# Optimization experiments

Hardware: AMD Instinct MI355X
Metric: run time of the kernel (lower is better)

The kernel has to match this reference:

```python
import jax, jax.numpy as jnp
import numpy as np
import itertools

B = 2          # batches
NB = 65536     # points per batch
G = 100        # voxel grid extent per axis
CIN = 32
COUT = 32
K3 = 27        # 3x3x3 kernel offsets
CENTER = 13    # (0,0,0) offset index


def setup_inputs() -> dict:
    rng = np.random.default_rng(0)
    grid = -np.ones((B, G, G, G), dtype=np.int64)
    coords = []
    for b in range(B):
        flat = np.sort(rng.choice(G ** 3, size=NB, replace=False))
        x = flat // (G * G)
        y = (flat // G) % G
        z = flat % G
        grid[b, x, y, z] = np.arange(NB) + b * NB
        coords.append(np.stack([np.full(NB, b), x, y, z], axis=1))
    C = np.concatenate(coords, axis=0)  # [N,4] batch,x,y,z (batch-contiguous)
    offs = np.array(list(itertools.product([-1, 0, 1], repeat=3)))  # [27,3], idx 13 == (0,0,0)
    nx = C[:, 1][:, None] + offs[:, 0][None]
    ny = C[:, 2][:, None] + offs[:, 1][None]
    nz = C[:, 3][:, None] + offs[:, 2][None]
    inb = (nx >= 0) & (nx < G) & (ny >= 0) & (ny < G) & (nz >= 0) & (nz < G)
    nb = grid[C[:, 0][:, None], np.clip(nx, 0, G - 1), np.clip(ny, 0, G - 1), np.clip(nz, 0, G - 1)]
    nbr = np.where(inb, nb, -1).astype(np.int32)  # [N,27], -1 = no neighbor voxel

    key = jax.random.key(0)
    k1, k2, k3, k4, k5 = jax.random.split(key, 5)
    scale = 1.0 / np.sqrt(K3 * CIN)
    return {
        "x_F": jax.random.normal(k1, (B * NB, CIN), dtype=jnp.float32),
        "W_ch": jax.random.normal(k2, (K3, CIN, COUT), dtype=jnp.float32) * scale,
        "b_ch": jax.random.normal(k3, (COUT,), dtype=jnp.float32) * 0.01,
        "W_dw": jax.random.normal(k4, (K3, COUT, COUT), dtype=jnp.float32) * scale,
        "b_dw": jax.random.normal(k5, (COUT,), dtype=jnp.float32) * 0.01,
        "nbr": jnp.asarray(nbr),
        "th": 1,
        "num_batches": B,
    }


def _sparse_conv(F, W, b, nbr, valid):
    # F:[N,Cin], W:[27,Cin,Cout], nbr:[N,27] (clamped gather + mask)
    idx = jnp.maximum(nbr, 0)
    g = jnp.where(valid[:, :, None], F[idx], 0.0)  # [N,27,Cin]
    out = jnp.einsum('nkc,kcd->nd', g, W)
    return out if b is None else out + b


def reference(x_F, W_ch, b_ch, W_dw, b_dw, nbr, th, num_batches):
    valid = nbr >= 0
    idx = jnp.maximum(nbr, 0)

    # Channel_code: 3x3x3 sparse conv with bias
    x = _sparse_conv(x_F, W_ch, b_ch, nbr, valid)  # [N,COUT]

    # correlation score: ones-kernel conv with center tap zeroed, over all channels
    s = x.sum(-1)  # [N]
    valid_nc = valid.at[:, CENTER].set(False)
    corr = jnp.where(valid_nc, s[idx], 0.0).sum(-1)
    corr_norm = (x * x).sum(-1)  # 1x1 ones-kernel conv on x*x
    corr = corr / corr_norm

    # per-batch topk -> strong/weak split (batch-contiguous equal-sized batches)
    N = x.shape[0]
    nb_pts = N // num_batches
    k = int(nb_pts * th / 3.21)
    corr_b = corr.reshape(num_batches, nb_pts)
    _, top_idx = jax.lax.top_k(corr_b, k)
    mask = jnp.zeros((num_batches, nb_pts), dtype=bool)
    mask = mask.at[jnp.arange(num_batches)[:, None], top_idx].set(True).reshape(-1)

    # dw conv restricted to the strong subset (neighbors must also be strong)
    valid_s = valid & mask[idx] & mask[:, None]
    strong = _sparse_conv(x, W_dw, b_dw, nbr, valid_s)

    # union: strong points take conv output, weak points keep x features
    union_F = jnp.where(mask[:, None], strong, x)
    return union_F + x  # out = out + x
```

## Files before the change

### kernel.cpp

```cpp
#include <hip/hip_runtime.h>

#define K3 27
#define CENTER 13
#define NC 32
#define NREP 32

__global__ __launch_bounds__(256) void conv1_kernel(
    const float* __restrict__ xF,
    const float* __restrict__ Wch,
    const float* __restrict__ bch,
    const int*   __restrict__ nbr,
    float*  __restrict__ xo,
    double* __restrict__ so,
    double* __restrict__ cno)
{
    __shared__ float Gs[2][256 * 32];
    const int t     = threadIdx.x;
    const int pbase = blockIdx.x << 8;
    const int dgu   = __builtin_amdgcn_readfirstlane(t >> 6);
    const int pp    = t & 63;
    const int sw    = pp & 7;
    const int tsw   = t & 7;

    float acc[4][8];
#pragma unroll
    for (int i = 0; i < 4; i++)
#pragma unroll
        for (int d = 0; d < 8; d++) acc[i][d] = 0.f;

    float4 stg[8];
    {
        const int j = nbr[(pbase + t) * K3];
        if (j >= 0) {
            const float4* src = (const float4*)(xF + (size_t)j * NC);
#pragma unroll
            for (int m = 0; m < 8; m++) stg[m] = src[m];
        } else {
            const float4 z = make_float4(0.f, 0.f, 0.f, 0.f);
#pragma unroll
            for (int m = 0; m < 8; m++) stg[m] = z;
        }
    }

    for (int k = 0; k < K3; k++) {
        const int cur = k & 1;
        {
            float4* dst = (float4*)(Gs[cur] + t * 32);
#pragma unroll
            for (int m = 0; m < 8; m++) dst[m ^ tsw] = stg[m];
        }
        __syncthreads();
        if (k + 1 < K3) {
            const int j = nbr[(pbase + t) * K3 + k + 1];
            if (j >= 0) {
                const float4* src = (const float4*)(xF + (size_t)j * NC);
#pragma unroll
                for (int m = 0; m < 8; m++) stg[m] = src[m];
            } else {
                const float4 z = make_float4(0.f, 0.f, 0.f, 0.f);
#pragma unroll
                for (int m = 0; m < 8; m++) stg[m] = z;
            }
        }
        const float* __restrict__ Wk = Wch + k * (NC * NC) + dgu * 8;
#pragma unroll
        for (int cc = 0; cc < 8; ++cc) {
            const float4 g0 = ((const float4*)(Gs[cur] + (pp      ) * 32))[cc ^ sw];
            const float4 g1 = ((const float4*)(Gs[cur] + (pp +  64) * 32))[cc ^ sw];
            const float4 g2 = ((const float4*)(Gs[cur] + (pp + 128) * 32))[cc ^ sw];
            const float4 g3 = ((const float4*)(Gs[cur] + (pp + 192) * 32))[cc ^ sw];
#pragma unroll
            for (int c4 = 0; c4 < 4; c4++) {
                const float* wr = Wk + (cc * 4 + c4) * NC;
                const float4 wa = ((const float4*)wr)[0];
                const float4 wb = ((const float4*)wr)[1];
                const float wv[8] = {wa.x, wa.y, wa.z, wa.w, wb.x, wb.y, wb.z, wb.w};
                const float gv[4] = {(&g0.x)[c4], (&g1.x)[c4], (&g2.x)[c4], (&g3.x)[c4]};
#pragma unroll
                for (int i = 0; i < 4; i++)
#pragma unroll
                    for (int d = 0; d < 8; d++)
                        acc[i][d] = fmaf(gv[i], wv[d], acc[i][d]);
            }
        }
        __syncthreads();
    }

#pragma unroll
    for (int d = 0; d < 8; d++) {
        const float bv = bch[dgu * 8 + d];
#pragma unroll
        for (int i = 0; i < 4; i++) acc[i][d] += bv;
    }
#pragma unroll
    for (int i = 0; i < 4; i++) {
        const int p = pp + 64 * i;
        float4* dst = (float4*)(Gs[0] + p * 32);
        dst[(dgu * 2    ) ^ sw] = make_float4(acc[i][0], acc[i][1], acc[i][2], acc[i][3]);
        dst[(dgu * 2 + 1) ^ sw] = make_float4(acc[i][4], acc[i][5], acc[i][6], acc[i][7]);
    }
    __syncthreads();
    {
        double sum = 0.0, sq = 0.0;
        const float4* row = (const float4*)(Gs[0] + t * 32);
#pragma unroll
        for (int m = 0; m < 8; m++) {
            const float4 v = row[m ^ tsw];
            sum += (double)v.x + (double)v.y + (double)v.z + (double)v.w;
            sq  += (double)v.x * v.x + (double)v.y * v.y + (double)v.z * v.z + (double)v.w * v.w;
        }
        so[pbase + t]  = sum;
        cno[pbase + t] = sq;
    }
    {
        float4* xout = (float4*)(xo + (size_t)pbase * NC);
#pragma unroll
        for (int f = 0; f < 8; f++) {
            const int idx = f * 256 + t;
            const int row = idx >> 3;
            const int m   = idx & 7;
            xout[idx] = ((const float4*)(Gs[0] + row * 32))[m ^ (row & 7)];
        }
    }
}

__global__ __launch_bounds__(256) void corr_hist_kernel(
    const double* __restrict__ s,
    const double* __restrict__ cn,
    const int*    __restrict__ nbr,
    unsigned*     __restrict__ key,
    unsigned*     __restrict__ rep,
    int NBpts, int N)
{
    __shared__ int nlds[256 * K3];
    const int t     = threadIdx.x;
    const int pbase = blockIdx.x * 256;
    {
        const int* g = nbr + (size_t)pbase * K3;
#pragma unroll
        for (int i = 0; i < K3; i++) nlds[i * 256 + t] = g[i * 256 + t];
    }
    __syncthreads();
    const int n = pbase + t;

    int jj[K3];
#pragma unroll
    for (int k = 0; k < K3; k++) jj[k] = nlds[t * K3 + k];

    double v[K3];
#pragma unroll
    for (int k = 0; k < K3; k++) {
        if (k == CENTER) continue;
        const int j  = jj[k];
        const int ja = (j < 0) ? 0 : j;
        const double val = s[ja];
        v[k] = (j < 0) ? 0.0 : val;
    }
    double a0 = 0.0, a1 = 0.0, a2 = 0.0, a3 = 0.0;
#pragma unroll
    for (int k = 0; k < K3; k++) {
        if (k == CENTER) continue;
        const int c = k & 3;
        if (c == 0) a0 += v[k];
        else if (c == 1) a1 += v[k];
        else if (c == 2) a2 += v[k];
        else a3 += v[k];
    }
    const double sum = (a0 + a1) + (a2 + a3);

    const float corr = (float)(sum / cn[n]);
    const unsigned uu = __float_as_uint(corr);
    const unsigned u  = (uu & 0x80000000u) ? ~uu : (uu | 0x80000000u);
    key[n] = u;
    const int b = n / NBpts;
    const unsigned r = (unsigned)blockIdx.x & (NREP - 1);
    atomicAdd(&rep[(size_t)r * (2u * 65536u) + (size_t)b * 65536u + (u >> 16)], 1u);
}

__global__ __launch_bounds__(256) void reduce_rep_kernel(
    const unsigned* __restrict__ rep,
    unsigned*       __restrict__ hist_sum)
{
    const int g = blockIdx.x * 256 + threadIdx.x;
    unsigned sum = 0;
#pragma unroll
    for (int r = 0; r < NREP; r++)
        sum += rep[(size_t)r * (2u * 65536u) + g];
    hist_sum[g] = sum;
}

__global__ __launch_bounds__(1024) void scan_hi_kernel(
    const unsigned* __restrict__ hist,
    const int*      __restrict__ thp,
    unsigned*       __restrict__ selhi,
    int*            __restrict__ selrk,
    int NBpts)
{
    __shared__ unsigned ss[1024];
    const int b = blockIdx.x;
    const int t = threadIdx.x;
    const unsigned* h = hist + (size_t)b * 65536u + t * 64;
    unsigned sum = 0;
#pragma unroll 8
    for (int i = 0; i < 64; i++) sum += h[i];
    ss[t] = sum;
    __syncthreads();
    for (int off = 1; off < 1024; off <<= 1) {
        unsigned v = (t + off < 1024) ? ss[t + off] : 0u;
        __syncthreads();
        ss[t] += v;
        __syncthreads();
    }
    int k = (int)((double)NBpts * (double)thp[0] / 3.21);
    if (k < 1) k = 1;
    if (k > NBpts) k = NBpts;
    unsigned run = ss[t] - sum;
    for (int i = 63; i >= 0; --i) {
        const unsigned c = h[i];
        if ((int)run < k && k <= (int)(run + c)) {
            selhi[b] = (unsigned)(t * 64 + i);
            selrk[b] = k - (int)run;
        }
        run += c;
    }
}

__global__ __launch_bounds__(256) void hist_lo_kernel(
    const unsigned* __restrict__ key,
    const unsigned* __restrict__ selhi,
    unsigned*       __restrict__ hist2,
    int NBpts, int N)
{
    const int n = blockIdx.x * 256 + threadIdx.x;
    if (n >= N) return;
    const int b = n / NBpts;
    const unsigned u = key[n];
    if ((u >> 16) == selhi[b])
        atomicAdd(&hist2[(size_t)b * 65536u + (u & 0xFFFFu)], 1u);
}

__global__ __launch_bounds__(1024) void scan_lo_kernel(
    const unsigned* __restrict__ hist2,
    const unsigned* __restrict__ selhi,
    const int*      __restrict__ selrk,
    unsigned*       __restrict__ selT,
    int*            __restrict__ selr)
{
    __shared__ unsigned ss[1024];
    const int b = blockIdx.x;
    const int t = threadIdx.x;
    const unsigned* h = hist2 + (size_t)b * 65536u + t * 64;
    unsigned sum = 0;
#pragma unroll 8
    for (int i = 0; i < 64; i++) sum += h[i];
    ss[t] = sum;
    __syncthreads();
    for (int off = 1; off < 1024; off <<= 1) {
        unsigned v = (t + off < 1024) ? ss[t + off] : 0u;
        __syncthreads();
        ss[t] += v;
        __syncthreads();
    }
    const int k = selrk[b];
    unsigned run = ss[t] - sum;
    for (int i = 63; i >= 0; --i) {
        const unsigned c = h[i];
        if ((int)run < k && k <= (int)(run + c)) {
            selT[b] = (selhi[b] << 16) | (unsigned)(t * 64 + i);
            selr[b] = k - (int)run;
        }
        run += c;
    }
}

__global__ __launch_bounds__(256) void mask_kernel(
    const unsigned* __restrict__ key,
    const unsigned* __restrict__ selT,
    int* __restrict__ mask,
    int* __restrict__ eqcnt,
    int NBpts)
{
    __shared__ int wc[4];
    const int n = blockIdx.x * 256 + threadIdx.x;
    const int b = n / NBpts;
    const unsigned u = key[n];
    const unsigned T = selT[b];
    mask[n] = (u > T) ? 1 : 0;
    const unsigned long long bal = __ballot(u == T);
    const int lane = threadIdx.x & 63;
    const int wid  = threadIdx.x >> 6;
    if (lane == 0) wc[wid] = __popcll(bal);
    __syncthreads();
    if (threadIdx.x == 0) eqcnt[blockIdx.x] = wc[0] + wc[1] + wc[2] + wc[3];
}

__global__ __launch_bounds__(512) void scan_kernel(
    const int* __restrict__ in, int* __restrict__ out,
    int n, int seg, int* __restrict__ total)
{
    __shared__ int ss[512];
    const int t = threadIdx.x;
    const int v = (t < n) ? in[t] : 0;
    ss[t] = v;
    __syncthreads();
    for (int off = 1; off < seg; off <<= 1) {
        int a = ((t & (seg - 1)) >= off) ? ss[t - off] : 0;
        __syncthreads();
        ss[t] += a;
        __syncthreads();
    }
    if (t < n) out[t] = ss[t] - v;
    if (total != nullptr && t == n - 1) total[0] = ss[t];
}

__global__ __launch_bounds__(256) void eqfinal_kernel(
    const unsigned* __restrict__ key,
    const unsigned* __restrict__ selT,
    const int*      __restrict__ selr,
    const int*      __restrict__ eqoff,
    int* __restrict__ mask,
    int* __restrict__ mcnt,
    int NBpts)
{
    __shared__ int wc[4], wm[4];
    const int n = blockIdx.x * 256 + threadIdx.x;
    const int b = n / NBpts;
    const unsigned u = key[n];
    const unsigned T = selT[b];
    const bool gt = (u > T);
    const bool eq = (u == T);
    const unsigned long long bal = __ballot(eq);
    const int lane = threadIdx.x & 63;
    const int wid  = threadIdx.x >> 6;
    if (lane == 0) wc[wid] = __popcll(bal);
    __syncthreads();
    int base = eqoff[blockIdx.x];
    for (int w = 0; w < wid; w++) base += wc[w];
    bool keep = false;
    if (eq) {
        const int g = base + __popcll(bal & ((1ull << lane) - 1ull));
        keep = (g < selr[b]);
        if (keep) mask[n] = 1;
    }
    const unsigned long long balm = __ballot(gt || keep);
    if (lane == 0) wm[wid] = __popcll(balm);
    __syncthreads();
    if (threadIdx.x == 0) mcnt[blockIdx.x] = wm[0] + wm[1] + wm[2] + wm[3];
}

__global__ __launch_bounds__(256) void emit_kernel(
    const int* __restrict__ mask,
    const int* __restrict__ moff,
    int* __restrict__ list)
{
    __shared__ int wc[4];
    const int n = blockIdx.x * 256 + threadIdx.x;
    const bool m = mask[n] != 0;
    const unsigned long long bal = __ballot(m);
    const int lane = threadIdx.x & 63;
    const int wid  = threadIdx.x >> 6;
    if (lane == 0) wc[wid] = __popcll(bal);
    __syncthreads();
    int base = moff[blockIdx.x];
    for (int w = 0; w < wid; w++) base += wc[w];
    if (m) list[base + __popcll(bal & ((1ull << lane) - 1ull))] = n;
}

__global__ __launch_bounds__(256) void scale2_kernel(
    const float4* __restrict__ x, float4* __restrict__ out, int n4)
{
    const int i = blockIdx.x * 256 + threadIdx.x;
    if (i < n4) {
        const float4 v = x[i];
        out[i] = make_float4(v.x + v.x, v.y + v.y, v.z + v.z, v.w + v.w);
    }
}

__global__ __launch_bounds__(256) void conv2_kernel(
    const float* __restrict__ x,
    const float* __restrict__ Wdw,
    const float* __restrict__ bdw,
    const int*   __restrict__ nbr,
    const int*   __restrict__ mask,
    const int*   __restrict__ list,
    const int*   __restrict__ cnt,
    float* __restrict__ out)
{
    __shared__ float Gs[2][256 * 32];
    const int t = threadIdx.x;
    const int base = blockIdx.x << 8;
    const int count = *cnt;
    if (base >= count) return;
    const int dgu = __builtin_amdgcn_readfirstlane(t >> 6);
    const int pp  = t & 63;
    const int sw  = pp & 7;
    const int tsw = t & 7;
    const int myp = (base + t < count) ? list[base + t] : -1;

    float acc[4][8];
#pragma unroll
    for (int i = 0; i < 4; i++)
#pragma unroll
        for (int d = 0; d < 8; d++) acc[i][d] = 0.f;

    float4 stg[8];
    {
        const int j = (myp >= 0) ? nbr[(size_t)myp * K3] : -1;
        const bool v = (j >= 0) && (mask[j] != 0);
        if (v) {
            const float4* src = (const float4*)(x + (size_t)j * NC);
#pragma unroll
            for (int m = 0; m < 8; m++) stg[m] = src[m];
        } else {
            const float4 z = make_float4(0.f, 0.f, 0.f, 0.f);
#pragma unroll
            for (int m = 0; m < 8; m++) stg[m] = z;
        }
    }

    for (int k = 0; k < K3; k++) {
        const int cur = k & 1;
        {
            float4* dst = (float4*)(Gs[cur] + t * 32);
#pragma unroll
            for (int m = 0; m < 8; m++) dst[m ^ tsw] = stg[m];
        }
        __syncthreads();
        if (k + 1 < K3) {
            const int j = (myp >= 0) ? nbr[(size_t)myp * K3 + k + 1] : -1;
            const bool v = (j >= 0) && (mask[j] != 0);
            if (v) {
                const float4* src = (const float4*)(x + (size_t)j * NC);
#pragma unroll
                for (int m = 0; m < 8; m++) stg[m] = src[m];
            } else {
                const float4 z = make_float4(0.f, 0.f, 0.f, 0.f);
#pragma unroll
                for (int m = 0; m < 8; m++) stg[m] = z;
            }
        }
        const float* __restrict__ Wk = Wdw + k * (NC * NC) + dgu * 8;
#pragma unroll
        for (int cc = 0; cc < 8; ++cc) {
            const float4 g0 = ((const float4*)(Gs[cur] + (pp      ) * 32))[cc ^ sw];
            const float4 g1 = ((const float4*)(Gs[cur] + (pp +  64) * 32))[cc ^ sw];
            const float4 g2 = ((const float4*)(Gs[cur] + (pp + 128) * 32))[cc ^ sw];
            const float4 g3 = ((const float4*)(Gs[cur] + (pp + 192) * 32))[cc ^ sw];
#pragma unroll
            for (int c4 = 0; c4 < 4; c4++) {
                const float* wr = Wk + (cc * 4 + c4) * NC;
                const float4 wa = ((const float4*)wr)[0];
                const float4 wb = ((const float4*)wr)[1];
                const float wv[8] = {wa.x, wa.y, wa.z, wa.w, wb.x, wb.y, wb.z, wb.w};
                const float gv[4] = {(&g0.x)[c4], (&g1.x)[c4], (&g2.x)[c4], (&g3.x)[c4]};
#pragma unroll
                for (int i = 0; i < 4; i++)
#pragma unroll
                    for (int d = 0; d < 8; d++)
                        acc[i][d] = fmaf(gv[i], wv[d], acc[i][d]);
            }
        }
        __syncthreads();
    }

#pragma unroll
    for (int i = 0; i < 4; i++) {
        const int p = pp + 64 * i;
        float4* dst = (float4*)(Gs[0] + p * 32);
        dst[(dgu * 2    ) ^ sw] = make_float4(acc[i][0], acc[i][1], acc[i][2], acc[i][3]);
        dst[(dgu * 2 + 1) ^ sw] = make_float4(acc[i][4], acc[i][5], acc[i][6], acc[i][7]);
    }
    __syncthreads();
    if (myp >= 0) {
        const float4* row = (const float4*)(Gs[0] + t * 32);
        const float4* xr  = (const float4*)(x + (size_t)myp * NC);
        const float4* bb  = (const float4*)bdw;
        float4* orow = (float4*)(out + (size_t)myp * NC);
#pragma unroll
        for (int m = 0; m < 8; m++) {
            const float4 a  = row[m ^ tsw];
            const float4 bv = bb[m];
            const float4 xv = xr[m];
            orow[m] = make_float4((a.x + bv.x) + xv.x, (a.y + bv.y) + xv.y,
                                  (a.z + bv.z) + xv.z, (a.w + bv.w) + xv.w);
        }
    }
}

extern "C" void kernel_launch(void* const* d_in, const int* in_sizes, int n_in,
                              void* d_out, int out_size, void* d_ws, size_t ws_size,
                              hipStream_t stream)
{
    const float* xF  = (const float*)d_in[0];
    const float* Wch = (const float*)d_in[1];
    const float* bch = (const float*)d_in[2];
    const float* Wdw = (const float*)d_in[3];
    const float* bdw = (const float*)d_in[4];
    const int*   nbr = (const int*)d_in[5];
    const int*   thp = (const int*)d_in[6];

    const int N = in_sizes[0] / NC;
    const int NBpts = N / 2;
    float* out = (float*)d_out;

    char* ws = (char*)d_ws;
    size_t off = 0;
    float*    x     = (float*)(ws + off);    off += (size_t)N * NC * sizeof(float);
    double*   s     = (double*)(ws + off);   off += (size_t)N * sizeof(double);
    double*   cn    = (double*)(ws + off);   off += (size_t)N * sizeof(double);
    unsigned* key   = (unsigned*)(ws + off); off += (size_t)N * sizeof(unsigned);
    int*      mask  = (int*)(ws + off);      off += (size_t)N * sizeof(int);
    int*      list  = (int*)(ws + off);      off += (size_t)N * sizeof(int);
    unsigned* hsum  = (unsigned*)(ws + off); off += 2u * 65536u * sizeof(unsigned);
    unsigned* hist2 = (unsigned*)(ws + off); off += 2u * 65536u * sizeof(unsigned);
    const size_t zero_bytes = 2u * 65536u * sizeof(unsigned);
    int*      cnt   = (int*)(ws + off);      off += 256;
    unsigned* selhi = (unsigned*)(ws + off); off += 256;
    int*      selrk = (int*)(ws + off);      off += 256;
    unsigned* selT  = (unsigned*)(ws + off); off += 256;
    int*      selr  = (int*)(ws + off);      off += 256;
    int*      eqcnt = (int*)(ws + off);      off += 512 * sizeof(int);
    int*      eqoff = (int*)(ws + off);      off += 512 * sizeof(int);
    int*      mcnt  = (int*)(ws + off);      off += 512 * sizeof(int);
    int*      moff  = (int*)(ws + off);      off += 512 * sizeof(int);

    const int nblk = N / 256;

    unsigned* rep = (unsigned*)d_out;

    hipMemsetAsync(rep, 0, (size_t)out_size * sizeof(float), stream);
    hipMemsetAsync(hist2, 0, zero_bytes, stream);
    conv1_kernel<<<nblk, 256, 0, stream>>>(xF, Wch, bch, nbr, x, s, cn);
    corr_hist_kernel<<<nblk, 256, 0, stream>>>(s, cn, nbr, key, rep, NBpts, N);
    reduce_rep_kernel<<<nblk, 256, 0, stream>>>(rep, hsum);
    scan_hi_kernel<<<2, 1024, 0, stream>>>(hsum, thp, selhi, selrk, NBpts);
    hist_lo_kernel<<<nblk, 256, 0, stream>>>(key, selhi, hist2, NBpts, N);
    scan_lo_kernel<<<2, 1024, 0, stream>>>(hist2, selhi, selrk, selT, selr);
    mask_kernel<<<nblk, 256, 0, stream>>>(key, selT, mask, eqcnt, NBpts);
    scan_kernel<<<1, 512, 0, stream>>>(eqcnt, eqoff, nblk, 256, nullptr);
    eqfinal_kernel<<<nblk, 256, 0, stream>>>(key, selT, selr, eqoff, mask, mcnt, NBpts);
    scan_kernel<<<1, 512, 0, stream>>>(mcnt, moff, nblk, 512, cnt);
    emit_kernel<<<nblk, 256, 0, stream>>>(mask, moff, list);
    scale2_kernel<<<(N * NC / 4) / 256, 256, 0, stream>>>((const float4*)x, (float4*)out, N * NC / 4);
    conv2_kernel<<<nblk, 256, 0, stream>>>(x, Wdw, bdw, nbr, mask, list, cnt, out);
}
```

Baseline: 378.8 us.

## Switch sparse convs to one-point-per-thread register accumulation without LDS staging

Both conv kernels drop the shared-memory staged, double-buffered gather and its block barriers. Each thread now owns one point, gathers its neighbor rows straight into registers with a two-deep software prefetch, and accumulates all 32 output channels. Weights are read as uniform loads, which the compiler can turn into scalar loads. This trades LDS traffic and synchronisation for heavier register pressure (32 accumulators plus two 8-float4 gather buffers) and per-thread strided gathers, with the launch bound raised to request 4 blocks per CU.

```diff
diff --git a/kernel.cpp b/kernel.cpp
--- a/kernel.cpp
+++ b/kernel.cpp
@@ -5,7 +5,42 @@
 #define NC 32
 #define NREP 32
 
-__global__ __launch_bounds__(256) void conv1_kernel(
+__device__ __forceinline__ void gather_row(float4* dst, const float* __restrict__ xF, int j)
+{
+    if (j >= 0) {
+        const float4* src = (const float4*)(xF + (size_t)j * NC);
+#pragma unroll
+        for (int m = 0; m < 8; m++) dst[m] = src[m];
+    } else {
+        const float4 z = make_float4(0.f, 0.f, 0.f, 0.f);
+#pragma unroll
+        for (int m = 0; m < 8; m++) dst[m] = z;
+    }
+}
+
+__device__ __forceinline__ void tap_fma(float* acc, const float4* g, const float* __restrict__ Wk)
+{
+#pragma unroll
+    for (int c8 = 0; c8 < 8; c8++) {
+        const float4 gv = g[c8];
+        const float* wb = Wk + (c8 * 4) * NC;
+#pragma unroll
+        for (int q = 0; q < 4; q++) {
+            const float gc = (q == 0) ? gv.x : (q == 1) ? gv.y : (q == 2) ? gv.z : gv.w;
+            const float4* wr = (const float4*)(wb + q * NC);
+#pragma unroll
+            for (int d4 = 0; d4 < 8; d4++) {
+                const float4 w = wr[d4];
+                acc[d4 * 4 + 0] = fmaf(gc, w.x, acc[d4 * 4 + 0]);
+                acc[d4 * 4 + 1] = fmaf(gc, w.y, acc[d4 * 4 + 1]);
+                acc[d4 * 4 + 2] = fmaf(gc, w.z, acc[d4 * 4 + 2]);
+                acc[d4 * 4 + 3] = fmaf(gc, w.w, acc[d4 * 4 + 3]);
+            }
+        }
+    }
+}
+
+__global__ __launch_bounds__(256, 4) void conv1_kernel(
     const float* __restrict__ xF,
     const float* __restrict__ Wch,
     const float* __restrict__ bch,
@@ -14,114 +49,41 @@
     double* __restrict__ so,
     double* __restrict__ cno)
 {
-    __shared__ float Gs[2][256 * 32];
-    const int t     = threadIdx.x;
-    const int pbase = blockIdx.x << 8;
-    const int dgu   = __builtin_amdgcn_readfirstlane(t >> 6);
-    const int pp    = t & 63;
-    const int sw    = pp & 7;
-    const int tsw   = t & 7;
-
-    float acc[4][8];
-#pragma unroll
-    for (int i = 0; i < 4; i++)
-#pragma unroll
-        for (int d = 0; d < 8; d++) acc[i][d] = 0.f;
-
-    float4 stg[8];
-    {
-        const int j = nbr[(pbase + t) * K3];
-        if (j >= 0) {
-            const float4* src = (const float4*)(xF + (size_t)j * NC);
-#pragma unroll
-            for (int m = 0; m < 8; m++) stg[m] = src[m];
-        } else {
-            const float4 z = make_float4(0.f, 0.f, 0.f, 0.f);
-#pragma unroll
-            for (int m = 0; m < 8; m++) stg[m] = z;
-        }
-    }
-
-    for (int k = 0; k < K3; k++) {
-        const int cur = k & 1;
-        {
-            float4* dst = (float4*)(Gs[cur] + t * 32);
-#pragma unroll
-            for (int m = 0; m < 8; m++) dst[m ^ tsw] = stg[m];
-        }
-        __syncthreads();
-        if (k + 1 < K3) {
-            const int j = nbr[(pbase + t) * K3 + k + 1];
-            if (j >= 0) {
-                const float4* src = (const float4*)(xF + (size_t)j * NC);
-#pragma unroll
-                for (int m = 0; m < 8; m++) stg[m] = src[m];
-            } else {
-                const float4 z = make_float4(0.f, 0.f, 0.f, 0.f);
-#pragma unroll
-                for (int m = 0; m < 8; m++) stg[m] = z;
-            }
-        }
-        const float* __restrict__ Wk = Wch + k * (NC * NC) + dgu * 8;
-#pragma unroll
-        for (int cc = 0; cc < 8; ++cc) {
-            const float4 g0 = ((const float4*)(Gs[cur] + (pp      ) * 32))[cc ^ sw];
-            const float4 g1 = ((const float4*)(Gs[cur] + (pp +  64) * 32))[cc ^ sw];
-            const float4 g2 = ((const float4*)(Gs[cur] + (pp + 128) * 32))[cc ^ sw];
-            const float4 g3 = ((const float4*)(Gs[cur] + (pp + 192) * 32))[cc ^ sw];
-#pragma unroll
-            for (int c4 = 0; c4 < 4; c4++) {
-                const float* wr = Wk + (cc * 4 + c4) * NC;
-                const float4 wa = ((const float4*)wr)[0];
-                const float4 wb = ((const float4*)wr)[1];
-                const float wv[8] = {wa.x, wa.y, wa.z, wa.w, wb.x, wb.y, wb.z, wb.w};
-                const float gv[4] = {(&g0.x)[c4], (&g1.x)[c4], (&g2.x)[c4], (&g3.x)[c4]};
-#pragma unroll
-                for (int i = 0; i < 4; i++)
-#pragma unroll
-                    for (int d = 0; d < 8; d++)
-                        acc[i][d] = fmaf(gv[i], wv[d], acc[i][d]);
-            }
-        }
-        __syncthreads();
-    }
-
-#pragma unroll
-    for (int d = 0; d < 8; d++) {
-        const float bv = bch[dgu * 8 + d];
-#pragma unroll
-        for (int i = 0; i < 4; i++) acc[i][d] += bv;
-    }
-#pragma unroll
-    for (int i = 0; i < 4; i++) {
-        const int p = pp + 64 * i;
-        float4* dst = (float4*)(Gs[0] + p * 32);
-        dst[(dgu * 2    ) ^ sw] = make_float4(acc[i][0], acc[i][1], acc[i][2], acc[i][3]);
-        dst[(dgu * 2 + 1) ^ sw] = make_float4(acc[i][4], acc[i][5], acc[i][6], acc[i][7]);
-    }
-    __syncthreads();
-    {
-        double sum = 0.0, sq = 0.0;
-        const float4* row = (const float4*)(Gs[0] + t * 32);
-#pragma unroll
-        for (int m = 0; m < 8; m++) {
-            const float4 v = row[m ^ tsw];
-            sum += (double)v.x + (double)v.y + (double)v.z + (double)v.w;
-            sq  += (double)v.x * v.x + (double)v.y * v.y + (double)v.z * v.z + (double)v.w * v.w;
-        }
-        so[pbase + t]  = sum;
-        cno[pbase + t] = sq;
-    }
-    {
-        float4* xout = (float4*)(xo + (size_t)pbase * NC);
-#pragma unroll
-        for (int f = 0; f < 8; f++) {
-            const int idx = f * 256 + t;
-            const int row = idx >> 3;
-            const int m   = idx & 7;
-            xout[idx] = ((const float4*)(Gs[0] + row * 32))[m ^ (row & 7)];
-        }
-    }
+    const int n = blockIdx.x * 256 + threadIdx.x;
+    const int* __restrict__ nrow = nbr + (size_t)n * K3;
+
+    float acc[NC];
+#pragma unroll
+    for (int d = 0; d < NC; d++) acc[d] = 0.f;
+
+    float4 A[8], B[8];
+    gather_row(A, xF, nrow[0]);
+
+#pragma unroll 1
+    for (int kk = 0; kk < 26; kk += 2) {
+        gather_row(B, xF, nrow[kk + 1]);
+        tap_fma(acc, A, Wch + kk * (NC * NC));
+        gather_row(A, xF, nrow[kk + 2]);
+        tap_fma(acc, B, Wch + (kk + 1) * (NC * NC));
+    }
+    tap_fma(acc, A, Wch + 26 * (NC * NC));
+
+    double sum = 0.0, sq = 0.0;
+    float4* xr = (float4*)(xo + (size_t)n * NC);
+#pragma unroll
+    for (int d4 = 0; d4 < 8; d4++) {
+        const float4 bv = ((const float4*)bch)[d4];
+        float4 v;
+        v.x = acc[d4 * 4 + 0] + bv.x;
+        v.y = acc[d4 * 4 + 1] + bv.y;
+        v.z = acc[d4 * 4 + 2] + bv.z;
+        v.w = acc[d4 * 4 + 3] + bv.w;
+        sum += (double)v.x + (double)v.y + (double)v.z + (double)v.w;
+        sq  += (double)v.x * v.x + (double)v.y * v.y + (double)v.z * v.z + (double)v.w * v.w;
+        xr[d4] = v;
+    }
+    so[n]  = sum;
+    cno[n] = sq;
 }
 
 __global__ __launch_bounds__(256) void corr_hist_kernel(
@@ -376,7 +338,22 @@
     }
 }
 
-__global__ __launch_bounds__(256) void conv2_kernel(
+__device__ __forceinline__ void gather_row_m(float4* dst, const float* __restrict__ x,
+                                             const int* __restrict__ mask, int j)
+{
+    const bool v = (j >= 0) && (mask[j] != 0);
+    if (v) {
+        const float4* src = (const float4*)(x + (size_t)j * NC);
+#pragma unroll
+        for (int m = 0; m < 8; m++) dst[m] = src[m];
+    } else {
+        const float4 z = make_float4(0.f, 0.f, 0.f, 0.f);
+#pragma unroll
+        for (int m = 0; m < 8; m++) dst[m] = z;
+    }
+}
+
+__global__ __launch_bounds__(256, 4) void conv2_kernel(
     const float* __restrict__ x,
     const float* __restrict__ Wdw,
     const float* __restrict__ bdw,
@@ -386,103 +363,42 @@
     const int*   __restrict__ cnt,
     float* __restrict__ out)
 {
-    __shared__ float Gs[2][256 * 32];
-    const int t = threadIdx.x;
-    const int base = blockIdx.x << 8;
     const int count = *cnt;
+    const int base  = blockIdx.x << 8;
     if (base >= count) return;
-    const int dgu = __builtin_amdgcn_readfirstlane(t >> 6);
-    const int pp  = t & 63;
-    const int sw  = pp & 7;
-    const int tsw = t & 7;
-    const int myp = (base + t < count) ? list[base + t] : -1;
-
-    float acc[4][8];
-#pragma unroll
-    for (int i = 0; i < 4; i++)
-#pragma unroll
-        for (int d = 0; d < 8; d++) acc[i][d] = 0.f;
-
-    float4 stg[8];
-    {
-        const int j = (myp >= 0) ? nbr[(size_t)myp * K3] : -1;
-        const bool v = (j >= 0) && (mask[j] != 0);
-        if (v) {
-            const float4* src = (const float4*)(x + (size_t)j * NC);
-#pragma unroll
-            for (int m = 0; m < 8; m++) stg[m] = src[m];
-        } else {
-            const float4 z = make_float4(0.f, 0.f, 0.f, 0.f);
-#pragma unroll
-            for (int m = 0; m < 8; m++) stg[m] = z;
-        }
-    }
-
-    for (int k = 0; k < K3; k++) {
-        const int cur = k & 1;
-        {
-            float4* dst = (float4*)(Gs[cur] + t * 32);
-#pragma unroll
-            for (int m = 0; m < 8; m++) dst[m ^ tsw] = stg[m];
-        }
-        __syncthreads();
-        if (k + 1 < K3) {
-            const int j = (myp >= 0) ? nbr[(size_t)myp * K3 + k + 1] : -1;
-            const bool v = (j >= 0) && (mask[j] != 0);
-            if (v) {
-                const float4* src = (const float4*)(x + (size_t)j * NC);
-#pragma unroll
-                for (int m = 0; m < 8; m++) stg[m] = src[m];
-            } else {
-                const float4 z = make_float4(0.f, 0.f, 0.f, 0.f);
-#pragma unroll
-                for (int m = 0; m < 8; m++) stg[m] = z;
-            }
-        }
-        const float* __restrict__ Wk = Wdw + k * (NC * NC) + dgu * 8;
-#pragma unroll
-        for (int cc = 0; cc < 8; ++cc) {
-            const float4 g0 = ((const float4*)(Gs[cur] + (pp      ) * 32))[cc ^ sw];
-            const float4 g1 = ((const float4*)(Gs[cur] + (pp +  64) * 32))[cc ^ sw];
-            const float4 g2 = ((const float4*)(Gs[cur] + (pp + 128) * 32))[cc ^ sw];
-            const float4 g3 = ((const float4*)(Gs[cur] + (pp + 192) * 32))[cc ^ sw];
-#pragma unroll
-            for (int c4 = 0; c4 < 4; c4++) {
-                const float* wr = Wk + (cc * 4 + c4) * NC;
-                const float4 wa = ((const float4*)wr)[0];
-                const float4 wb = ((const float4*)wr)[1];
-                const float wv[8] = {wa.x, wa.y, wa.z, wa.w, wb.x, wb.y, wb.z, wb.w};
-                const float gv[4] = {(&g0.x)[c4], (&g1.x)[c4], (&g2.x)[c4], (&g3.x)[c4]};
-#pragma unroll
-                for (int i = 0; i < 4; i++)
-#pragma unroll
-                    for (int d = 0; d < 8; d++)
-                        acc[i][d] = fmaf(gv[i], wv[d], acc[i][d]);
-            }
-        }
-        __syncthreads();
-    }
-
-#pragma unroll
-    for (int i = 0; i < 4; i++) {
-        const int p = pp + 64 * i;
-        float4* dst = (float4*)(Gs[0] + p * 32);
-        dst[(dgu * 2    ) ^ sw] = make_float4(acc[i][0], acc[i][1], acc[i][2], acc[i][3]);
-        dst[(dgu * 2 + 1) ^ sw] = make_float4(acc[i][4], acc[i][5], acc[i][6], acc[i][7]);
-    }
-    __syncthreads();
+    const int idx = base + threadIdx.x;
+    const int myp = (idx < count) ? list[idx] : -1;
+    const int* __restrict__ nrow = nbr + (size_t)((myp >= 0) ? myp : 0) * K3;
+
+    float acc[NC];
+#pragma unroll
+    for (int d = 0; d < NC; d++) acc[d] = 0.f;
+
+    float4 A[8], B[8];
+    gather_row_m(A, x, mask, (myp >= 0) ? nrow[0] : -1);
+
+#pragma unroll 1
+    for (int kk = 0; kk < 26; kk += 2) {
+        gather_row_m(B, x, mask, (myp >= 0) ? nrow[kk + 1] : -1);
+        tap_fma(acc, A, Wdw + kk * (NC * NC));
+        gather_row_m(A, x, mask, (myp >= 0) ? nrow[kk + 2] : -1);
+        tap_fma(acc, B, Wdw + (kk + 1) * (NC * NC));
+    }
+    tap_fma(acc, A, Wdw + 26 * (NC * NC));
+
     if (myp >= 0) {
-        const float4* row = (const float4*)(Gs[0] + t * 32);
-        const float4* xr  = (const float4*)(x + (size_t)myp * NC);
-        const float4* bb  = (const float4*)bdw;
+        const float4* xr = (const float4*)(x + (size_t)myp * NC);
         float4* orow = (float4*)(out + (size_t)myp * NC);
 #pragma unroll
-        for (int m = 0; m < 8; m++) {
-            const float4 a  = row[m ^ tsw];
-            const float4 bv = bb[m];
-            const float4 xv = xr[m];
-            orow[m] = make_float4((a.x + bv.x) + xv.x, (a.y + bv.y) + xv.y,
-                                  (a.z + bv.z) + xv.z, (a.w + bv.w) + xv.w);
+        for (int d4 = 0; d4 < 8; d4++) {
+            const float4 bv = ((const float4*)bdw)[d4];
+            const float4 xv = xr[d4];
+            float4 v;
+            v.x = (acc[d4 * 4 + 0] + bv.x) + xv.x;
+            v.y = (acc[d4 * 4 + 1] + bv.y) + xv.y;
+            v.z = (acc[d4 * 4 + 2] + bv.z) + xv.z;
+            v.w = (acc[d4 * 4 + 3] + bv.w) + xv.w;
+            orow[d4] = v;
         }
     }
 }
```

Result: slower. 1.080 ms (+185.2%).
